# Kernel optimization log

Measured on AMD Instinct MI355X. Metric: run time of the kernel, lower is better.

Reference implementation:

```python
import jax, jax.numpy as jnp
import numpy as np

EMBED_DIM = 768
NUM_HEADS = 12
D_K = EMBED_DIM // NUM_HEADS


def setup_inputs() -> dict:
    key = jax.random.key(0)
    k_x, k_qkv, k_out_w, k_out_b = jax.random.split(key, 4)
    B, S = 1, 4096
    x = jax.random.normal(k_x, (B, S, EMBED_DIM), dtype=jnp.float32)
    # nn.Linear(embed_dim, 3*embed_dim, bias=False): weight [3E, E], y = x @ W^T
    scale_qkv = 1.0 / np.sqrt(EMBED_DIM)
    w_qkv = jax.random.uniform(k_qkv, (3 * EMBED_DIM, EMBED_DIM), dtype=jnp.float32,
                               minval=-scale_qkv, maxval=scale_qkv)
    w_out = jax.random.uniform(k_out_w, (EMBED_DIM, EMBED_DIM), dtype=jnp.float32,
                               minval=-scale_qkv, maxval=scale_qkv)
    b_out = jax.random.uniform(k_out_b, (EMBED_DIM,), dtype=jnp.float32,
                               minval=-scale_qkv, maxval=scale_qkv)
    return {"x": x, "w_qkv": w_qkv, "w_out": w_out, "b_out": b_out}


def reference(x, w_qkv, w_out, b_out):
    B, S, E = x.shape
    H, Dk = NUM_HEADS, D_K
    # qkv projection: [B,S,3E] -> [3,B,H,S,Dk]
    qkv = jnp.einsum('bse,fe->bsf', x, w_qkv)
    qkv = qkv.reshape(B, S, 3, H, Dk).transpose(2, 0, 3, 1, 4)
    q, k, v = qkv[0], qkv[1], qkv[2]
    # scaled dot-product attention, full [B,H,S,S] scores (naive, faithful)
    scores = jnp.einsum('bhsd,bhtd->bhst', q, k) / jnp.sqrt(jnp.float32(Dk))
    attn = jax.nn.softmax(scores, axis=-1)
    # dropout is identity in eval/deterministic baseline
    out = jnp.einsum('bhst,bhtd->bhsd', attn, v)
    out = out.transpose(0, 2, 1, 3).reshape(B, S, E)
    return jnp.einsum('bse,fe->bsf', out, w_out) + b_out
```

## Files before the change

### kernel.cpp

```cpp
#include <hip/hip_runtime.h>
#include <hip/hip_bf16.h>

constexpr int S_LEN   = 4096;
constexpr int EMB     = 768;
constexpr int NH      = 12;
constexpr int DK      = 64;
constexpr int QKV_DIM = 3 * EMB;
constexpr int NSPLIT  = 2;
constexpr int TSPLIT  = S_LEN / NSPLIT;

typedef short bf16x8 __attribute__((ext_vector_type(8)));
typedef float f32x4  __attribute__((ext_vector_type(4)));
typedef unsigned short u16;

__device__ inline u16 f2bf(float x) {
  unsigned u = __float_as_uint(x);
  unsigned r = u + 0x7fffu + ((u >> 16) & 1u);
  return (u16)(r >> 16);
}
__device__ inline float bf2f(u16 h) {
  return __uint_as_float(((unsigned)h) << 16);
}

__device__ inline void gld16(unsigned* lds, const unsigned* g) {
  __builtin_amdgcn_global_load_lds(
      (const __attribute__((address_space(1))) unsigned*)g,
      (__attribute__((address_space(3))) unsigned*)lds, 16, 0, 0);
}

__device__ inline float fast_exp2(float x) {
  float r;
  asm("v_exp_f32 %0, %1" : "=v"(r) : "v"(x));
  return r;
}

#define LOG2E 1.4426950408889634f

__global__ __launch_bounds__(256) void cast_bf16_fused(
    const float* __restrict__ s0, u16* __restrict__ d0, int n0,
    const float* __restrict__ s1, u16* __restrict__ d1, int n1,
    const float* __restrict__ s2, u16* __restrict__ d2, int n2)
{
  const float* src; u16* dst; int n8, b0, nb;
  if (blockIdx.x < 512)      { src = s0; dst = d0; n8 = n0; b0 = 0;   nb = 512; }
  else if (blockIdx.x < 768) { src = s1; dst = d1; n8 = n1; b0 = 512; nb = 256; }
  else                       { src = s2; dst = d2; n8 = n2; b0 = 768; nb = 128; }
  for (int i = (blockIdx.x - b0) * 256 + threadIdx.x; i < n8; i += nb * 256) {
    float4 a = reinterpret_cast<const float4*>(src)[2 * i + 0];
    float4 b = reinterpret_cast<const float4*>(src)[2 * i + 1];
    ushort4 h0, h1;
    const float* ap = reinterpret_cast<const float*>(&a);
    const float* bp = reinterpret_cast<const float*>(&b);
#pragma unroll
    for (int j = 0; j < 4; ++j) {
      reinterpret_cast<u16*>(&h0)[j] = f2bf(ap[j]);
      reinterpret_cast<u16*>(&h1)[j] = f2bf(bp[j]);
    }
    reinterpret_cast<ushort4*>(dst)[2 * i + 0] = h0;
    reinterpret_cast<ushort4*>(dst)[2 * i + 1] = h1;
  }
}

template<int MODE>
__global__ __launch_bounds__(256) void gemm_bf16_nt(
    const u16* __restrict__ A, const u16* __restrict__ B,
    const float* __restrict__ bias,
    u16* __restrict__ Cb, float* __restrict__ Cf,
    int M, int N, int K)
{
  __shared__ __align__(16) u16 sA[128 * 64];
  __shared__ __align__(16) u16 sB[128 * 64];

  const int tid  = threadIdx.x;
  const int w    = tid >> 6;
  const int l    = tid & 63;
  const int lg   = l >> 4;
  const int lr   = l & 15;
  const int wr   = w >> 1;
  const int wc   = w & 1;
  const int brow = blockIdx.x * 128;
  const int bcol = blockIdx.y * 128;

  const int srow = l >> 3;
  const int sslot = l & 7;

  f32x4 acc[4][4] = {};

  for (int k0 = 0; k0 < K; k0 += 64) {
#pragma unroll
    for (int cc = 0; cc < 4; ++cc) {
      int c = w * 4 + cc;
      int row = c * 8 + srow;
      int kswz = (sslot ^ (row & 7)) * 8;
      size_t aoff = (size_t)(brow + row) * K + k0 + kswz;
      size_t boff = (size_t)(bcol + row) * K + k0 + kswz;
      gld16((unsigned*)(sA + c * 512), (const unsigned*)(A + aoff));
      gld16((unsigned*)(sB + c * 512), (const unsigned*)(B + boff));
    }
    __syncthreads();

#pragma unroll
    for (int ks = 0; ks < 2; ++ks) {
      bf16x8 fa[4], fb[4];
#pragma unroll
      for (int i = 0; i < 4; ++i) {
        int arow = wr * 64 + i * 16 + lr;
        int brow_ = wc * 64 + i * 16 + lr;
        fa[i] = *reinterpret_cast<const bf16x8*>(
            &sA[arow * 64 + (((lg + 4 * ks) ^ (arow & 7)) << 3)]);
        fb[i] = *reinterpret_cast<const bf16x8*>(
            &sB[brow_ * 64 + (((lg + 4 * ks) ^ (brow_ & 7)) << 3)]);
      }
#pragma unroll
      for (int mi = 0; mi < 4; ++mi)
#pragma unroll
        for (int ni = 0; ni < 4; ++ni)
          acc[mi][ni] = __builtin_amdgcn_mfma_f32_16x16x32_bf16(
              fa[mi], fb[ni], acc[mi][ni], 0, 0, 0);
    }
    __syncthreads();
  }

  if (MODE == 0) {
    const float qscale = (bcol < EMB) ? 0.125f * LOG2E : 1.0f;
#pragma unroll
    for (int mi = 0; mi < 4; ++mi)
#pragma unroll
      for (int ni = 0; ni < 4; ++ni)
#pragma unroll
        for (int r = 0; r < 4; ++r) {
          size_t m = brow + wr * 64 + mi * 16 + 4 * lg + r;
          size_t n = bcol + wc * 64 + ni * 16 + lr;
          Cb[m * N + n] = f2bf(acc[mi][ni][r] * qscale);
        }
  } else {
#pragma unroll
    for (int mi = 0; mi < 4; ++mi)
#pragma unroll
      for (int ni = 0; ni < 4; ++ni)
#pragma unroll
        for (int r = 0; r < 4; ++r) {
          size_t m = brow + wr * 64 + mi * 16 + 4 * lg + r;
          size_t n = bcol + wc * 64 + ni * 16 + lr;
          Cf[m * N + n] = acc[mi][ni][r] + bias[n];
        }
  }
}

__device__ inline int key7(int row) { return (row ^ (row >> 3)) & 7; }
__device__ inline int swz16(int row, int s) {
  return row * 64 + ((s ^ key7(row)) << 3);
}
__device__ inline int swz32(int row, int p) {
  return row * 32 + ((((p >> 2) ^ key7(row)) << 2) | (p & 3));
}

__global__ __launch_bounds__(256, 3) void flash_split(
    const u16* __restrict__ qkv, float* __restrict__ Sp,
    float* __restrict__ lp)
{
  __shared__ __align__(16) u16 Ks[2][64 * 64];
  __shared__ __align__(16) u16 Vt[2][64 * 64];
  __shared__ __align__(16) u16 Ps[4][32 * 64];

  const int tid = threadIdx.x;
  const int w   = tid >> 6;
  const int l   = tid & 63;
  const int lg  = l >> 4;
  const int lr  = l & 15;

  const int bid   = blockIdx.x;
  const int sbid  = (bid & 7) * 96 + (bid >> 3);
  const int split = sbid & 1;
  const int qb    = ((sbid >> 1) & 31) * 128;
  const int h     = sbid >> 6;
  const int tbeg  = split * TSPLIT;

  unsigned* Pw = (unsigned*)Ps[w];

  const int tq  = tid >> 3;
  const int vgs = tid & 7;

  int kfO[4][2], paO[2][2], pwO[2][4], vcO[8];
#pragma unroll
  for (int tt = 0; tt < 4; ++tt)
#pragma unroll
    for (int ks = 0; ks < 2; ++ks)
      kfO[tt][ks] = swz16(tt * 16 + lr, 4 * ks + lg);
#pragma unroll
  for (int qf = 0; qf < 2; ++qf) {
#pragma unroll
    for (int ks = 0; ks < 2; ++ks)
      paO[qf][ks] = swz16(qf * 16 + lr, 4 * ks + lg);
#pragma unroll
    for (int tt = 0; tt < 4; ++tt)
      pwO[qf][tt] = swz32(qf * 16 + lr, 8 * tt + 2 * lg);
  }
#pragma unroll
  for (int j = 0; j < 8; ++j)
    vcO[j] = swz32(vgs * 8 + j, tq);

  const int kt0 = tid >> 3, kg0 = tid & 7;
  const int kgo0 = kt0 * QKV_DIM + ((kg0 ^ key7(kt0)) << 3);
  const int kgo1 = (kt0 + 32) * QKV_DIM + ((kg0 ^ key7(kt0 + 32)) << 3);

  const u16* kg = qkv + EMB + h * DK + (size_t)tbeg * QKV_DIM;
  const u16* vg = qkv + 2 * EMB + h * DK +
                  ((size_t)tbeg + 2 * tq) * QKV_DIM + vgs * 8;

  bf16x8 qfr[2][2];
#pragma unroll
  for (int qf = 0; qf < 2; ++qf)
#pragma unroll
    for (int ks = 0; ks < 2; ++ks)
      qfr[qf][ks] = *reinterpret_cast<const bf16x8*>(
          qkv + (size_t)(qb + w * 32 + qf * 16 + lr) * QKV_DIM + h * DK + ks * 32 + lg * 8);

  bf16x8 ones;
#pragma unroll
  for (int i = 0; i < 8; ++i) ones[i] = (short)0x3F80;

  f32x4 acc[2][4] = {};
  f32x4 lacc[2]   = {};
  uint4 vr0, vr1;

  gld16((unsigned*)(Ks[0] + tid * 8),        (const unsigned*)(kg + kgo0));
  gld16((unsigned*)(Ks[0] + 2048 + tid * 8), (const unsigned*)(kg + kgo1));
  vr0 = *reinterpret_cast<const uint4*>(vg);
  vr1 = *reinterpret_cast<const uint4*>(vg + QKV_DIM);

  constexpr int NT = TSPLIT / 64;

#define FL_ITER(CUR, IT)                                                       \
  {                                                                            \
                              \
    {                                                                          \
      unsigned* vdst = (unsigned*)Vt[CUR];                                     \
      const unsigned* a0 = reinterpret_cast<const unsigned*>(&vr0);            \
      const unsigned* a1 = reinterpret_cast<const unsigned*>(&vr1);            \
      _Pragma("unroll")                                                        \
      for (int j = 0; j < 8; ++j) {                                            \
        unsigned sel = (j & 1) ? 0x07060302u : 0x05040100u;                    \
        vdst[vcO[j]] = __builtin_amdgcn_perm(a1[j >> 1], a0[j >> 1], sel);     \
      }                                                                        \
    }                                                                          \
    __syncthreads();                                                           \
                                         \
    if ((IT) + 1 < NT) {                                                       \
      kg += 64 * QKV_DIM;                                                      \
      vg += 64 * QKV_DIM;                                                      \
      gld16((unsigned*)(Ks[(CUR) ^ 1] + tid * 8),                              \
            (const unsigned*)(kg + kgo0));                                     \
      gld16((unsigned*)(Ks[(CUR) ^ 1] + 2048 + tid * 8),                       \
            (const unsigned*)(kg + kgo1));                                     \
      vr0 = *reinterpret_cast<const uint4*>(vg);                               \
      vr1 = *reinterpret_cast<const uint4*>(vg + QKV_DIM);                     \
    }                                                                          \
                                              \
    {                                                                          \
      bf16x8 kf[4][2];                                                         \
      _Pragma("unroll")                                                        \
      for (int tt = 0; tt < 4; ++tt) {                                         \
        kf[tt][0] = *reinterpret_cast<const bf16x8*>(&Ks[CUR][kfO[tt][0]]);    \
        kf[tt][1] = *reinterpret_cast<const bf16x8*>(&Ks[CUR][kfO[tt][1]]);    \
      }                                                                        \
      _Pragma("unroll")                                                        \
      for (int qf = 0; qf < 2; ++qf) {                                         \
        f32x4 s[4] = {};                                                       \
        __builtin_amdgcn_s_setprio(1);                                         \
        _Pragma("unroll")                                                      \
        for (int tt = 0; tt < 4; ++tt) {                                       \
          s[tt] = __builtin_amdgcn_mfma_f32_16x16x32_bf16(                     \
              kf[tt][0], qfr[qf][0], s[tt], 0, 0, 0);                          \
          s[tt] = __builtin_amdgcn_mfma_f32_16x16x32_bf16(                     \
              kf[tt][1], qfr[qf][1], s[tt], 0, 0, 0);                          \
        }                                                                      \
        __builtin_amdgcn_s_setprio(0);                                         \
        _Pragma("unroll")                                                      \
        for (int tt = 0; tt < 4; ++tt) {                                       \
          float p0 = fast_exp2(s[tt][0]);                                      \
          float p1 = fast_exp2(s[tt][1]);                                      \
          float p2 = fast_exp2(s[tt][2]);                                      \
          float p3 = fast_exp2(s[tt][3]);                                      \
          uint2 pv;                                                            \
          pv.x = __builtin_amdgcn_perm(__float_as_uint(p1),                    \
                                       __float_as_uint(p0), 0x07060302u);      \
          pv.y = __builtin_amdgcn_perm(__float_as_uint(p3),                    \
                                       __float_as_uint(p2), 0x07060302u);      \
          *reinterpret_cast<uint2*>(&Pw[pwO[qf][tt]]) = pv;                    \
        }                                                                      \
      }                                                                        \
      __builtin_amdgcn_s_setprio(1);                                           \
      _Pragma("unroll")                                                        \
      for (int ks = 0; ks < 2; ++ks) {                                         \
        bf16x8 pa[2];                                                          \
        pa[0] = *reinterpret_cast<const bf16x8*>(&Ps[w][paO[0][ks]]);          \
        pa[1] = *reinterpret_cast<const bf16x8*>(&Ps[w][paO[1][ks]]);          \
        lacc[0] = __builtin_amdgcn_mfma_f32_16x16x32_bf16(                     \
            ones, pa[0], lacc[0], 0, 0, 0);                                    \
        lacc[1] = __builtin_amdgcn_mfma_f32_16x16x32_bf16(                     \
            ones, pa[1], lacc[1], 0, 0, 0);                                    \
        _Pragma("unroll")                                                      \
        for (int dt = 0; dt < 4; ++dt) {                                       \
          bf16x8 vf = *reinterpret_cast<const bf16x8*>(&Vt[CUR][kfO[dt][ks]]); \
          acc[0][dt] = __builtin_amdgcn_mfma_f32_16x16x32_bf16(                \
              vf, pa[0], acc[0][dt], 0, 0, 0);                                 \
          acc[1][dt] = __builtin_amdgcn_mfma_f32_16x16x32_bf16(                \
              vf, pa[1], acc[1][dt], 0, 0, 0);                                 \
        }                                                                      \
      }                                                                        \
      __builtin_amdgcn_s_setprio(0);                                           \
    }                                                                          \
  }

  for (int it = 0; it < NT; it += 2) {
    FL_ITER(0, it);
    FL_ITER(1, it + 1);
  }
#undef FL_ITER

#pragma unroll
  for (int qf = 0; qf < 2; ++qf) {
    int q = qb + w * 32 + qf * 16 + lr;
    size_t base = ((size_t)split * S_LEN + q) * EMB + h * DK;
#pragma unroll
    for (int dt = 0; dt < 4; ++dt)
      *reinterpret_cast<float4*>(&Sp[base + dt * 16 + 4 * lg]) =
          *reinterpret_cast<float4*>(&acc[qf][dt]);
    if (lg == 0)
      lp[((size_t)split * NH + h) * S_LEN + q] = lacc[qf][0];
  }
}

__global__ __launch_bounds__(256) void combine_splits(
    const float* __restrict__ Sp, const float* __restrict__ lp,
    u16* __restrict__ ao)
{
  constexpr int N4 = S_LEN * EMB / 4;
  for (int i = blockIdx.x * 256 + threadIdx.x; i < N4; i += gridDim.x * 256) {
    int q = i / 192;
    int t = i - q * 192;
    int h = t >> 4;
    float la = lp[(size_t)h * S_LEN + q];
    float lb = lp[(size_t)(NH + h) * S_LEN + q];
    float inv = 1.0f / (la + lb);
    float4 s0 = reinterpret_cast<const float4*>(Sp)[i];
    float4 s1 = reinterpret_cast<const float4*>(Sp)[N4 + i];
    ushort4 o;
    o.x = f2bf((s0.x + s1.x) * inv);
    o.y = f2bf((s0.y + s1.y) * inv);
    o.z = f2bf((s0.z + s1.z) * inv);
    o.w = f2bf((s0.w + s1.w) * inv);
    reinterpret_cast<ushort4*>(ao)[i] = o;
  }
}

extern "C" void kernel_launch(void* const* d_in, const int* in_sizes, int n_in,
                              void* d_out, int out_size, void* d_ws, size_t ws_size,
                              hipStream_t stream) {
  const float* x     = (const float*)d_in[0];
  const float* w_qkv = (const float*)d_in[1];
  const float* w_out = (const float*)d_in[2];
  const float* b_out = (const float*)d_in[3];
  float* out = (float*)d_out;

  constexpr size_t NX  = (size_t)S_LEN * EMB;
  constexpr size_t NWQ = (size_t)QKV_DIM * EMB;
  constexpr size_t NWO = (size_t)EMB * EMB;
  constexpr size_t NQ  = (size_t)S_LEN * QKV_DIM;

  u16* xb    = (u16*)d_ws;
  u16* wqb   = xb + NX;
  u16* wob   = wqb + NWQ;
  u16* qkvb  = wob + NWO;
  float* Sp  = (float*)(qkvb + NQ);
  float* lp  = Sp + (size_t)NSPLIT * S_LEN * EMB;
  u16* aob   = xb;

  dim3 blk(256);

  cast_bf16_fused<<<dim3(896), blk, 0, stream>>>(
      x, xb, (int)(NX / 8), w_qkv, wqb, (int)(NWQ / 8), w_out, wob, (int)(NWO / 8));

  gemm_bf16_nt<0><<<dim3(S_LEN / 128, QKV_DIM / 128), blk, 0, stream>>>(
      xb, wqb, nullptr, qkvb, nullptr, S_LEN, QKV_DIM, EMB);

  flash_split<<<dim3(768), blk, 0, stream>>>(qkvb, Sp, lp);
  combine_splits<<<dim3(1024), blk, 0, stream>>>(Sp, lp, aob);

  gemm_bf16_nt<1><<<dim3(S_LEN / 128, EMB / 128), blk, 0, stream>>>(
      aob, wob, b_out, nullptr, out, S_LEN, EMB, EMB);
}
```

Baseline: 121.7 us.

## Fuse split-combine normalization into output projection GEMM A-tile load

```diff
diff --git a/kernel.cpp b/kernel.cpp
--- a/kernel.cpp
+++ b/kernel.cpp
@@ -61,12 +61,9 @@
   }
 }
 
-template<int MODE>
-__global__ __launch_bounds__(256) void gemm_bf16_nt(
+__global__ __launch_bounds__(256) void gemm_qkv(
     const u16* __restrict__ A, const u16* __restrict__ B,
-    const float* __restrict__ bias,
-    u16* __restrict__ Cb, float* __restrict__ Cf,
-    int M, int N, int K)
+    u16* __restrict__ Cb, int M, int N, int K)
 {
   __shared__ __align__(16) u16 sA[128 * 64];
   __shared__ __align__(16) u16 sB[128 * 64];
@@ -121,30 +118,113 @@
     __syncthreads();
   }
 
-  if (MODE == 0) {
-    const float qscale = (bcol < EMB) ? 0.125f * LOG2E : 1.0f;
-#pragma unroll
-    for (int mi = 0; mi < 4; ++mi)
-#pragma unroll
-      for (int ni = 0; ni < 4; ++ni)
-#pragma unroll
-        for (int r = 0; r < 4; ++r) {
-          size_t m = brow + wr * 64 + mi * 16 + 4 * lg + r;
-          size_t n = bcol + wc * 64 + ni * 16 + lr;
-          Cb[m * N + n] = f2bf(acc[mi][ni][r] * qscale);
-        }
-  } else {
-#pragma unroll
-    for (int mi = 0; mi < 4; ++mi)
-#pragma unroll
-      for (int ni = 0; ni < 4; ++ni)
-#pragma unroll
-        for (int r = 0; r < 4; ++r) {
-          size_t m = brow + wr * 64 + mi * 16 + 4 * lg + r;
-          size_t n = bcol + wc * 64 + ni * 16 + lr;
-          Cf[m * N + n] = acc[mi][ni][r] + bias[n];
-        }
-  }
+  const float qscale = (bcol < EMB) ? 0.125f * LOG2E : 1.0f;
+#pragma unroll
+  for (int mi = 0; mi < 4; ++mi)
+#pragma unroll
+    for (int ni = 0; ni < 4; ++ni)
+#pragma unroll
+      for (int r = 0; r < 4; ++r) {
+        size_t m = brow + wr * 64 + mi * 16 + 4 * lg + r;
+        size_t n = bcol + wc * 64 + ni * 16 + lr;
+        Cb[m * N + n] = f2bf(acc[mi][ni][r] * qscale);
+      }
+}
+
+__global__ __launch_bounds__(256) void gemm_out_fused(
+    const float* __restrict__ Sp, const float* __restrict__ lp,
+    const u16* __restrict__ B, const float* __restrict__ bias,
+    float* __restrict__ Cf)
+{
+  __shared__ __align__(16) u16 sA[128 * 64];
+  __shared__ __align__(16) u16 sB[128 * 64];
+
+  constexpr int K = EMB, N = EMB;
+  constexpr size_t NSP = (size_t)S_LEN * EMB;
+
+  const int tid  = threadIdx.x;
+  const int w    = tid >> 6;
+  const int l    = tid & 63;
+  const int lg   = l >> 4;
+  const int lr   = l & 15;
+  const int wr   = w >> 1;
+  const int wc   = w & 1;
+  const int brow = blockIdx.x * 128;
+  const int bcol = blockIdx.y * 128;
+
+  const int srow = l >> 3;
+  const int sslot = l & 7;
+
+  f32x4 acc[4][4] = {};
+
+  for (int k0 = 0; k0 < K; k0 += 64) {
+    const int h = k0 >> 6;
+#pragma unroll
+    for (int cc = 0; cc < 4; ++cc) {
+      int c = w * 4 + cc;
+      int lrow = c * 8 + srow;
+      int row  = brow + lrow;
+      int kswz = (sslot ^ (lrow & 7)) * 8;
+      const float* p0 = Sp + (size_t)row * EMB + k0 + kswz;
+      float4 a0 = *reinterpret_cast<const float4*>(p0);
+      float4 a1 = *reinterpret_cast<const float4*>(p0 + 4);
+      float4 b0 = *reinterpret_cast<const float4*>(p0 + NSP);
+      float4 b1 = *reinterpret_cast<const float4*>(p0 + NSP + 4);
+      float inv = 1.0f / (lp[(size_t)h * S_LEN + row] +
+                          lp[(size_t)(NH + h) * S_LEN + row]);
+      ushort4 h0, h1;
+      const float* ap = reinterpret_cast<const float*>(&a0);
+      const float* bp = reinterpret_cast<const float*>(&b0);
+      const float* cp = reinterpret_cast<const float*>(&a1);
+      const float* dp = reinterpret_cast<const float*>(&b1);
+#pragma unroll
+      for (int j = 0; j < 4; ++j) {
+        reinterpret_cast<u16*>(&h0)[j] = f2bf((ap[j] + bp[j]) * inv);
+        reinterpret_cast<u16*>(&h1)[j] = f2bf((cp[j] + dp[j]) * inv);
+      }
+      uint4 pack;
+      pack.x = (unsigned)h0.x | ((unsigned)h0.y << 16);
+      pack.y = (unsigned)h0.z | ((unsigned)h0.w << 16);
+      pack.z = (unsigned)h1.x | ((unsigned)h1.y << 16);
+      pack.w = (unsigned)h1.z | ((unsigned)h1.w << 16);
+      *reinterpret_cast<uint4*>(&sA[lrow * 64 + sslot * 8]) = pack;
+      size_t boff = (size_t)(bcol + lrow) * K + k0 + kswz;
+      gld16((unsigned*)(sB + c * 512), (const unsigned*)(B + boff));
+    }
+    __syncthreads();
+
+#pragma unroll
+    for (int ks = 0; ks < 2; ++ks) {
+      bf16x8 fa[4], fb[4];
+#pragma unroll
+      for (int i = 0; i < 4; ++i) {
+        int arow = wr * 64 + i * 16 + lr;
+        int brow_ = wc * 64 + i * 16 + lr;
+        fa[i] = *reinterpret_cast<const bf16x8*>(
+            &sA[arow * 64 + (((lg + 4 * ks) ^ (arow & 7)) << 3)]);
+        fb[i] = *reinterpret_cast<const bf16x8*>(
+            &sB[brow_ * 64 + (((lg + 4 * ks) ^ (brow_ & 7)) << 3)]);
+      }
+#pragma unroll
+      for (int mi = 0; mi < 4; ++mi)
+#pragma unroll
+        for (int ni = 0; ni < 4; ++ni)
+          acc[mi][ni] = __builtin_amdgcn_mfma_f32_16x16x32_bf16(
+              fa[mi], fb[ni], acc[mi][ni], 0, 0, 0);
+    }
+    __syncthreads();
+  }
+
+#pragma unroll
+  for (int mi = 0; mi < 4; ++mi)
+#pragma unroll
+    for (int ni = 0; ni < 4; ++ni)
+#pragma unroll
+      for (int r = 0; r < 4; ++r) {
+        size_t m = brow + wr * 64 + mi * 16 + 4 * lg + r;
+        size_t n = bcol + wc * 64 + ni * 16 + lr;
+        Cf[m * N + n] = acc[mi][ni][r] + bias[n];
+      }
 }
 
 __device__ inline int key7(int row) { return (row ^ (row >> 3)) & 7; }
@@ -332,29 +412,6 @@
   }
 }
 
-__global__ __launch_bounds__(256) void combine_splits(
-    const float* __restrict__ Sp, const float* __restrict__ lp,
-    u16* __restrict__ ao)
-{
-  constexpr int N4 = S_LEN * EMB / 4;
-  for (int i = blockIdx.x * 256 + threadIdx.x; i < N4; i += gridDim.x * 256) {
-    int q = i / 192;
-    int t = i - q * 192;
-    int h = t >> 4;
-    float la = lp[(size_t)h * S_LEN + q];
-    float lb = lp[(size_t)(NH + h) * S_LEN + q];
-    float inv = 1.0f / (la + lb);
-    float4 s0 = reinterpret_cast<const float4*>(Sp)[i];
-    float4 s1 = reinterpret_cast<const float4*>(Sp)[N4 + i];
-    ushort4 o;
-    o.x = f2bf((s0.x + s1.x) * inv);
-    o.y = f2bf((s0.y + s1.y) * inv);
-    o.z = f2bf((s0.z + s1.z) * inv);
-    o.w = f2bf((s0.w + s1.w) * inv);
-    reinterpret_cast<ushort4*>(ao)[i] = o;
-  }
-}
-
 extern "C" void kernel_launch(void* const* d_in, const int* in_sizes, int n_in,
                               void* d_out, int out_size, void* d_ws, size_t ws_size,
                               hipStream_t stream) {
@@ -375,19 +432,17 @@
   u16* qkvb  = wob + NWO;
   float* Sp  = (float*)(qkvb + NQ);
   float* lp  = Sp + (size_t)NSPLIT * S_LEN * EMB;
-  u16* aob   = xb;
 
   dim3 blk(256);
 
   cast_bf16_fused<<<dim3(896), blk, 0, stream>>>(
       x, xb, (int)(NX / 8), w_qkv, wqb, (int)(NWQ / 8), w_out, wob, (int)(NWO / 8));
 
-  gemm_bf16_nt<0><<<dim3(S_LEN / 128, QKV_DIM / 128), blk, 0, stream>>>(
-      xb, wqb, nullptr, qkvb, nullptr, S_LEN, QKV_DIM, EMB);
+  gemm_qkv<<<dim3(S_LEN / 128, QKV_DIM / 128), blk, 0, stream>>>(
+      xb, wqb, qkvb, S_LEN, QKV_DIM, EMB);
 
   flash_split<<<dim3(768), blk, 0, stream>>>(qkvb, Sp, lp);
-  combine_splits<<<dim3(1024), blk, 0, stream>>>(Sp, lp, aob);
-
-  gemm_bf16_nt<1><<<dim3(S_LEN / 128, EMB / 128), blk, 0, stream>>>(
-      aob, wob, b_out, nullptr, out, S_LEN, EMB, EMB);
-}
+
+  gemm_out_fused<<<dim3(S_LEN / 128, EMB / 128), blk, 0, stream>>>(
+      Sp, lp, wob, b_out, out);
+}
```

New measurement: 127.2 us. +4.5%, slower.
